# Performance work log

Hardware: AMD Instinct MI355X
Metric: run time of the kernel (lower is better)

## Reference

```python
import jax, jax.numpy as jnp
import numpy as np

N_NODES = 40000
N_EDGES = 640000
D = 128
BN_EPS = 1e-5
GATE_EPS = 1e-6


def _linear_params(key, d_in, d_out):
    kw, kb = jax.random.split(key)
    bound = 1.0 / np.sqrt(d_in)
    W = jax.random.uniform(kw, (d_out, d_in), jnp.float32, -bound, bound)
    b = jax.random.uniform(kb, (d_out,), jnp.float32, -bound, bound)
    return W, b


def setup_inputs() -> dict:
    key = jax.random.key(0)
    ks = jax.random.split(key, 8)
    x = jax.random.normal(ks[0], (N_NODES, D), jnp.float32)
    edge_index = jax.random.randint(ks[1], (2, N_EDGES), 0, N_NODES, jnp.int64)
    edge_attr = jax.random.normal(ks[2], (N_EDGES, D), jnp.float32)
    W_src_gate, b_src_gate = _linear_params(ks[3], D, D)
    W_dst_gate, b_dst_gate = _linear_params(ks[4], D, D)
    W_edge_gate, b_edge_gate = _linear_params(ks[5], D, D)
    W_src_update, b_src_update = _linear_params(ks[6], D, D)
    W_dst_update, b_dst_update = _linear_params(ks[7], D, D)
    return dict(
        x=x, edge_index=edge_index, edge_attr=edge_attr,
        W_src_gate=W_src_gate, b_src_gate=b_src_gate,
        W_dst_gate=W_dst_gate, b_dst_gate=b_dst_gate,
        W_edge_gate=W_edge_gate, b_edge_gate=b_edge_gate,
        W_src_update=W_src_update, b_src_update=b_src_update,
        W_dst_update=W_dst_update, b_dst_update=b_dst_update,
        bn_nodes_gamma=jnp.ones((D,), jnp.float32), bn_nodes_beta=jnp.zeros((D,), jnp.float32),
        bn_edges_gamma=jnp.ones((D,), jnp.float32), bn_edges_beta=jnp.zeros((D,), jnp.float32),
    )


def _batch_norm(z, gamma, beta):
    # training-mode BN: batch mean, biased variance (torch semantics)
    mean = jnp.mean(z, axis=0)
    var = jnp.mean(jnp.square(z - mean), axis=0)
    return gamma * (z - mean) * jax.lax.rsqrt(var + BN_EPS) + beta


def reference(x, edge_index, edge_attr,
              W_src_gate, b_src_gate, W_dst_gate, b_dst_gate,
              W_edge_gate, b_edge_gate, W_src_update, b_src_update,
              W_dst_update, b_dst_update,
              bn_nodes_gamma, bn_nodes_beta, bn_edges_gamma, bn_edges_beta):
    row, col = edge_index[0], edge_index[1]
    num_nodes = x.shape[0]
    x_row = x[row]                      # [E, D] gather
    x_col = x[col]                      # [E, D] gather
    e_src = x_row @ W_src_gate.T + b_src_gate
    e_dst = x_col @ W_dst_gate.T + b_dst_gate
    m = e_src + e_dst + edge_attr @ W_edge_gate.T + b_edge_gate  # [E, D]
    sigma = jax.nn.sigmoid(m)
    h_weighted = (x_col @ W_dst_update.T + b_dst_update) * sigma
    h_sum = jax.ops.segment_sum(h_weighted, col, num_segments=num_nodes)
    sigma_sum = jax.ops.segment_sum(sigma, col, num_segments=num_nodes)
    h_normalized = h_sum / (sigma_sum + GATE_EPS)
    x_new = x @ W_src_update.T + b_src_update + h_normalized
    x_new = jax.nn.softplus(_batch_norm(x_new, bn_nodes_gamma, bn_nodes_beta))
    y_new = jax.nn.softplus(_batch_norm(m, bn_edges_gamma, bn_edges_beta))
    x_new = x + x_new          # residual
    y_new = edge_attr + y_new  # residual
    return (x_new, y_new)
```

## Files before the change

### kernel.cpp

```cpp
#include <hip/hip_runtime.h>

#define NN 40000
#define NE 640000

typedef unsigned short u16;
typedef unsigned int u32;
typedef __attribute__((ext_vector_type(4))) float f32x4;
typedef __attribute__((ext_vector_type(4))) float fv4;
typedef __attribute__((ext_vector_type(4))) u32 uv4;
typedef __attribute__((ext_vector_type(8))) __bf16 bf16x8;

#define LSTR 132
#define TPW 8

__device__ __forceinline__ float bf2f(u16 u) { return __uint_as_float(((u32)u) << 16); }
__device__ __forceinline__ u16 f2bf(float f) {
  u32 u = __float_as_uint(f);
  u32 r = 0x7fffu + ((u >> 16) & 1u);
  return (u16)((u + r) >> 16);
}
__device__ __forceinline__ float splus(float v) {
  return fmaxf(v, 0.0f) + __logf(1.0f + __expf(-fabsf(v)));
}

__global__ void sniff_k(const u32* __restrict__ gamma, const u32* __restrict__ eidx,
                        u32* __restrict__ flags) {
  if (threadIdx.x == 0) {
    flags[0] = (gamma[0] == 0x3F803F80u) ? 1u : 0u;
    u32 odd = eidx[1] | eidx[3] | eidx[5] | eidx[7] |
              eidx[9] | eidx[11] | eidx[13] | eidx[15];
    flags[1] = (odd == 0u) ? 1u : 0u;
  }
}

__device__ __forceinline__ int load_col(const void* eidx, int e, u32 i64) {
  int nc = i64 ? (int)((const u32*)eidx)[2 * ((size_t)NE + e)]
               : ((const int*)eidx)[NE + e];
  return min(max(nc, 0), NN - 1);
}
__device__ __forceinline__ int load_row(const void* eidx, int e, u32 i64) {
  int nr = i64 ? (int)((const u32*)eidx)[2 * (size_t)e]
               : ((const int*)eidx)[e];
  return min(max(nr, 0), NN - 1);
}

__global__ __launch_bounds__(256) void wconv5_k(
    const float* __restrict__ W0, const float* __restrict__ W1,
    const float* __restrict__ W2, const float* __restrict__ W3,
    const float* __restrict__ W4, u16* __restrict__ out) {
  int i = blockIdx.x * 256 + threadIdx.x;
  int mtx = blockIdx.y;
  const float* W = (mtx == 0) ? W0 : (mtx == 1) ? W1 : (mtx == 2) ? W2
                 : (mtx == 3) ? W3 : W4;
  out[mtx * 16384 + i] = f2bf(W[i]);
}

__global__ __launch_bounds__(256) void hist_k(const void* __restrict__ eidx,
                                              u32* __restrict__ cnt,
                                              const u32* __restrict__ flags) {
  int e = blockIdx.x * 256 + threadIdx.x;
  atomicAdd(&cnt[load_col(eidx, e, flags[1])], 1u);
}

__device__ __forceinline__ bf16x8 a_frag(const float* __restrict__ row, int kbase) {
  float4 f0 = *(const float4*)(row + kbase);
  float4 f1 = *(const float4*)(row + kbase + 4);
  bf16x8 a;
  a[0] = (__bf16)f0.x; a[1] = (__bf16)f0.y; a[2] = (__bf16)f0.z; a[3] = (__bf16)f0.w;
  a[4] = (__bf16)f1.x; a[5] = (__bf16)f1.y; a[6] = (__bf16)f1.z; a[7] = (__bf16)f1.w;
  return a;
}

__device__ __forceinline__ bf16x8 cvt8v(fv4 a, fv4 b) {
  bf16x8 r;
  r[0] = (__bf16)a[0]; r[1] = (__bf16)a[1]; r[2] = (__bf16)a[2]; r[3] = (__bf16)a[3];
  r[4] = (__bf16)b[0]; r[5] = (__bf16)b[1]; r[6] = (__bf16)b[2]; r[7] = (__bf16)b[3];
  return r;
}

__device__ __forceinline__ void gemm16(const bf16x8 af[4], const u16* __restrict__ Wb,
                                       const float* __restrict__ bias, int lane,
                                       f32x4 acc[8]) {
  int l15 = lane & 15, lk = lane >> 4;
#pragma unroll
  for (int n = 0; n < 8; ++n) {
    float bv = bias[n * 16 + l15];
    acc[n] = (f32x4){bv, bv, bv, bv};
  }
#pragma unroll
  for (int n = 0; n < 8; ++n) {
    const u16* bp = Wb + (size_t)(n * 16 + l15) * 128 + lk * 8;
#pragma unroll
    for (int k = 0; k < 4; ++k) {
      bf16x8 b = *(const bf16x8*)(bp + 32 * k);
      acc[n] = __builtin_amdgcn_mfma_f32_16x16x32_bf16(af[k], b, acc[n], 0, 0, 0);
    }
  }
}

__device__ __forceinline__ void store_tile(u16* __restrict__ out, int m0, int lane,
                                           const f32x4 acc[8]) {
  int l15 = lane & 15, lk = lane >> 4;
#pragma unroll
  for (int n = 0; n < 8; ++n)
#pragma unroll
    for (int r = 0; r < 4; ++r)
      out[(size_t)(m0 + lk * 4 + r) * 128 + n * 16 + l15] = f2bf(acc[n][r]);
}

__global__ __launch_bounds__(256) void node_gemm_k(
    const float* __restrict__ x, const u16* __restrict__ Wb,
    const float* __restrict__ B0, const float* __restrict__ B1,
    const float* __restrict__ B2, const float* __restrict__ B3,
    const u32* __restrict__ cnt,
    u16* __restrict__ o0, u16* __restrict__ o1,
    u16* __restrict__ o2, u16* __restrict__ o3,
    float* __restrict__ statsg) {
  __shared__ float red[256];
  int tid = threadIdx.x, lane = tid & 63, w = tid >> 6;
  for (int i = tid; i < 256; i += 256) red[i] = 0.f;
  __syncthreads();
  int m0 = blockIdx.x * 64 + w * 16;
  int l15 = lane & 15, lk = lane >> 4;
  const float* arow = x + (size_t)(m0 + l15) * 128;
  bf16x8 af[4];
#pragma unroll
  for (int k = 0; k < 4; ++k) af[k] = a_frag(arow, 32 * k + 8 * lk);
  f32x4 acc[8], accd[8];
  gemm16(af, Wb + 0 * 16384, B0, lane, acc);  store_tile(o0, m0, lane, acc);
  gemm16(af, Wb + 1 * 16384, B1, lane, acc);  store_tile(o1, m0, lane, acc);
  gemm16(af, Wb + 2 * 16384, B2, lane, accd); store_tile(o2, m0, lane, accd);
  gemm16(af, Wb + 3 * 16384, B3, lane, acc);  store_tile(o3, m0, lane, acc);
  float g[4];
#pragma unroll
  for (int r = 0; r < 4; ++r) g[r] = (cnt[m0 + lk * 4 + r] != 0u) ? 1.0f : 0.0f;
#pragma unroll
  for (int n = 0; n < 8; ++n) {
    float a1 = 0.f, a2 = 0.f;
#pragma unroll
    for (int r = 0; r < 4; ++r) {
      float zv = acc[n][r] + g[r] * accd[n][r];
      a1 += zv;
      a2 = fmaf(zv, zv, a2);
    }
    a1 += __shfl_xor(a1, 16); a1 += __shfl_xor(a1, 32);
    a2 += __shfl_xor(a2, 16); a2 += __shfl_xor(a2, 32);
    if (lk == 0) {
      atomicAdd(&red[n * 16 + l15], a1);
      atomicAdd(&red[128 + n * 16 + l15], a2);
    }
  }
  __syncthreads();
  for (int i = tid; i < 256; i += 256) atomicAdd(&statsg[256 + i], red[i]);
}

__global__ __launch_bounds__(256, 2) void edge_gemm_k(
    const float* __restrict__ ea, const u16* __restrict__ Wgb,
    const float* __restrict__ Bg,
    const u16* __restrict__ g_src, const u16* __restrict__ g_dst,
    const void* __restrict__ eidx,
    u16* __restrict__ mge, float* __restrict__ statsg,
    const u32* __restrict__ flags) {
  __shared__ __align__(16) char gbuf[4][16 * LSTR * 4];
  __shared__ __align__(16) u16 Wl[16384];
  int tid = threadIdx.x, lane = tid & 63, w = tid >> 6;
  int l15 = lane & 15, lk = lane >> 4;
  int el = lane >> 2, c4 = lane & 3;
  u32 i64 = flags[1];

  {
    const u32* Wg32 = (const u32*)Wgb;
    u32* Wl32 = (u32*)Wl;
#pragma unroll
    for (int j = 0; j < 32; ++j) {
      int i2 = tid + 256 * j;
      int r = i2 >> 6, c2 = i2 & 63;
      int g = c2 >> 2, win = c2 & 3;
      Wl32[r * 64 + (((g ^ ((r & 7) << 1)) << 2) | win)] = Wg32[i2];
    }
  }
  __syncthreads();

  float* gt = (float*)gbuf[w];
  u16*   mt = (u16*)gbuf[w];
  int sw = (l15 & 7) << 1;

  float bias[8];
#pragma unroll
  for (int n = 0; n < 8; ++n) bias[n] = Bg[n * 16 + l15];

  float e1[8] = {0.f, 0.f, 0.f, 0.f, 0.f, 0.f, 0.f, 0.f};
  float e2[8] = {0.f, 0.f, 0.f, 0.f, 0.f, 0.f, 0.f, 0.f};

  int base = (blockIdx.x * 4 + w) * (TPW * 16);
  const float* aptr = ea + (size_t)(base + l15) * 128 + 8 * lk;

  int rowc = load_row(eidx, base + el, i64);
  int colc = load_col(eidx, base + el, i64);
  fv4 tmp[8];
#pragma unroll
  for (int k = 0; k < 4; ++k) {
    tmp[2 * k]     = *(const fv4*)(aptr + 32 * k);
    tmp[2 * k + 1] = *(const fv4*)(aptr + 32 * k + 4);
  }
  uv4 gsv[2][4], gdv[2][4];
#pragma unroll
  for (int it = 0; it < 4; ++it) {
    gsv[0][it] = *(const uv4*)(g_src + (size_t)rowc * 128 + c4 * 8 + it * 32);
    gdv[0][it] = *(const uv4*)(g_dst + (size_t)colc * 128 + c4 * 8 + it * 32);
  }
  int rown = load_row(eidx, base + 16 + el, i64);
  int coln = load_col(eidx, base + 16 + el, i64);
  bf16x8 af[4];
#pragma unroll
  for (int k = 0; k < 4; ++k) af[k] = cvt8v(tmp[2 * k], tmp[2 * k + 1]);

#pragma unroll
  for (int t = 0; t < TPW; ++t) {
    int cur = t & 1, nxt = cur ^ 1;
    int e0 = base + t * 16;
    if (t + 1 < TPW) {
      const float* anx = aptr + (size_t)(t + 1) * 16 * 128;
#pragma unroll
      for (int k = 0; k < 4; ++k) {
        tmp[2 * k]     = *(const fv4*)(anx + 32 * k);
        tmp[2 * k + 1] = *(const fv4*)(anx + 32 * k + 4);
      }
    }
    if (t + 1 < TPW) {
#pragma unroll
      for (int it = 0; it < 4; ++it) {
        gsv[nxt][it] = *(const uv4*)(g_src + (size_t)rown * 128 + c4 * 8 + it * 32);
        gdv[nxt][it] = *(const uv4*)(g_dst + (size_t)coln * 128 + c4 * 8 + it * 32);
      }
    }
    int rn2 = rown, cn2 = coln;
    if (t + 2 < TPW) {
      rn2 = load_row(eidx, base + (t + 2) * 16 + el, i64);
      cn2 = load_col(eidx, base + (t + 2) * 16 + el, i64);
    }
    f32x4 acc[8];
#pragma unroll
    for (int n = 0; n < 8; ++n)
      acc[n] = (f32x4){bias[n], bias[n], bias[n], bias[n]};
#pragma unroll
    for (int n = 0; n < 8; ++n)
#pragma unroll
      for (int k = 0; k < 4; ++k) {
        bf16x8 b = *(const bf16x8*)(Wl + ((n * 16 + l15) << 7) +
                                    (((lk + 4 * k) ^ sw) << 3));
        acc[n] = __builtin_amdgcn_mfma_f32_16x16x32_bf16(af[k], b, acc[n], 0, 0, 0);
      }
#pragma unroll
    for (int it = 0; it < 4; ++it) {
      const u16* sp = (const u16*)&gsv[cur][it];
      const u16* dp = (const u16*)&gdv[cur][it];
      fv4 lo, hi;
#pragma unroll
      for (int j = 0; j < 4; ++j) lo[j] = bf2f(sp[j]) + bf2f(dp[j]);
#pragma unroll
      for (int j = 0; j < 4; ++j) hi[j] = bf2f(sp[4 + j]) + bf2f(dp[4 + j]);
      int ch = c4 + 4 * it;
      *(fv4*)(gt + el * LSTR + ch * 8)     = lo;
      *(fv4*)(gt + el * LSTR + ch * 8 + 4) = hi;
    }
    float g32[8][4];
#pragma unroll
    for (int n = 0; n < 8; ++n)
#pragma unroll
      for (int r = 0; r < 4; ++r)
        g32[n][r] = gt[(lk * 4 + r) * LSTR + n * 16 + l15];
    __builtin_amdgcn_sched_barrier(0);
#pragma unroll
    for (int n = 0; n < 8; ++n)
#pragma unroll
      for (int r = 0; r < 4; ++r) {
        float mv = acc[n][r] + g32[n][r];
        e1[n] += mv;
        e2[n] = fmaf(mv, mv, e2[n]);
        mt[(lk * 4 + r) * LSTR + n * 16 + l15] = f2bf(mv);
      }
#pragma unroll
    for (int it = 0; it < 4; ++it) {
      int ch = c4 + 4 * it;
      uint4 v = *(const uint4*)(mt + el * LSTR + ch * 8);
      *(uint4*)(mge + (size_t)(e0 + el) * 128 + ch * 8) = v;
    }
    if (t + 1 < TPW) {
#pragma unroll
      for (int k = 0; k < 4; ++k) af[k] = cvt8v(tmp[2 * k], tmp[2 * k + 1]);
    }
    rown = rn2; coln = cn2;
  }
#pragma unroll
  for (int n = 0; n < 8; ++n) {
    float s1 = e1[n], s2 = e2[n];
    s1 += __shfl_xor(s1, 16); s1 += __shfl_xor(s1, 32);
    s2 += __shfl_xor(s2, 16); s2 += __shfl_xor(s2, 32);
    if (lk == 0) {
      atomicAdd(&statsg[n * 16 + l15], s1);
      atomicAdd(&statsg[128 + n * 16 + l15], s2);
    }
  }
}

__global__ void stats_fin_k(const float* __restrict__ es1, const float* __restrict__ es2,
                            const float* __restrict__ ns1, const float* __restrict__ ns2,
                            const float* __restrict__ eg_, const float* __restrict__ eb_,
                            const float* __restrict__ ng_, const float* __restrict__ nb_,
                            float* __restrict__ params) {
  int d = threadIdx.x;
  float em = es1[d] * (1.0f / NE);
  float ev = fmaxf(es2[d] * (1.0f / NE) - em * em, 0.0f);
  float esc = eg_[d] * rsqrtf(ev + 1e-5f);
  params[d] = esc;
  params[128 + d] = eb_[d] - em * esc;
  float nm = ns1[d] * (1.0f / NN);
  float nv = fmaxf(ns2[d] * (1.0f / NN) - nm * nm, 0.0f);
  float nsc = ng_[d] * rsqrtf(nv + 1e-5f);
  params[256 + d] = nsc;
  params[384 + d] = nb_[d] - nm * nsc;
}

__global__ __launch_bounds__(256) void node_fin2_k(
    const float* __restrict__ x, const u16* __restrict__ us,
    const u16* __restrict__ ud, const u32* __restrict__ cnt,
    const float* __restrict__ params, float* __restrict__ out) {
  size_t t = (size_t)blockIdx.x * 256 + threadIdx.x;
  size_t base = t * 8;
  int d0 = (int)(base & 127);
  int n = (int)(t >> 4);
  float g = (cnt[n] != 0u) ? 1.0f : 0.0f;
  float4 xa = *(const float4*)(x + base);
  float4 xb = *(const float4*)(x + base + 4);
  float xv[8] = {xa.x, xa.y, xa.z, xa.w, xb.x, xb.y, xb.z, xb.w};
  uint4 usv = *(const uint4*)(us + base);
  uint4 udv = *(const uint4*)(ud + base);
  const u16* up = (const u16*)&usv;
  const u16* dp = (const u16*)&udv;
  float o[8];
#pragma unroll
  for (int j = 0; j < 8; ++j) {
    float z = bf2f(up[j]) + g * bf2f(dp[j]);
    float bnv = z * params[256 + d0 + j] + params[384 + d0 + j];
    o[j] = xv[j] + splus(bnv);
  }
  *(float4*)(out + base) = make_float4(o[0], o[1], o[2], o[3]);
  *(float4*)(out + base + 4) = make_float4(o[4], o[5], o[6], o[7]);
}

__global__ __launch_bounds__(256) void edge_fin_k(
    const float* __restrict__ edge_attr, const u16* __restrict__ mge,
    const float* __restrict__ params, float* __restrict__ out) {
  size_t t = (size_t)blockIdx.x * 256 + threadIdx.x;
  size_t base = t * 8;
  int d0 = (int)(base & 127);
  float4 ea = *(const float4*)(edge_attr + base);
  float4 eb = *(const float4*)(edge_attr + base + 4);
  float ev[8] = {ea.x, ea.y, ea.z, ea.w, eb.x, eb.y, eb.z, eb.w};
  uint4 mv_ = *(const uint4*)(mge + base);
  const u16* mp = (const u16*)&mv_;
  float o[8];
#pragma unroll
  for (int j = 0; j < 8; ++j) {
    float m = bf2f(mp[j]);
    float bnv = m * params[d0 + j] + params[128 + d0 + j];
    o[j] = ev[j] + splus(bnv);
  }
  *(float4*)(out + base) = make_float4(o[0], o[1], o[2], o[3]);
  *(float4*)(out + base + 4) = make_float4(o[4], o[5], o[6], o[7]);
}

extern "C" void kernel_launch(void* const* d_in, const int* in_sizes, int n_in,
                              void* d_out, int out_size, void* d_ws, size_t ws_size,
                              hipStream_t stream) {
  const float* x        = (const float*)d_in[0];
  const void*  eidx     = d_in[1];
  const float* edge_att = (const float*)d_in[2];
  const float* Wsg = (const float*)d_in[3];  const float* bsg = (const float*)d_in[4];
  const float* Wdg = (const float*)d_in[5];  const float* bdg = (const float*)d_in[6];
  const float* Weg = (const float*)d_in[7];  const float* beg = (const float*)d_in[8];
  const float* Wsu = (const float*)d_in[9];  const float* bsu = (const float*)d_in[10];
  const float* Wdu = (const float*)d_in[11]; const float* bdu = (const float*)d_in[12];
  const float* bng = (const float*)d_in[13]; const float* bnb = (const float*)d_in[14];
  const float* beg_g = (const float*)d_in[15]; const float* beb = (const float*)d_in[16];

  char* ws = (char*)d_ws;
  u16*   g_src  = (u16*)(ws + 0);
  u16*   g_dst  = (u16*)(ws + 10240000);
  u16*   u_dst  = (u16*)(ws + 20480000);
  u16*   u_src  = (u16*)(ws + 30720000);
  float* stats  = (float*)(ws + 40960000);
  u32*   flags  = (u32*)(ws + 40964096);
  u16*   wbuf   = (u16*)(ws + 40968192);
  u32*   cnt    = (u32*)(ws + 41132032);
  u16*   mge    = (u16*)(ws + 41292032);

  hipMemsetAsync(stats, 0, 4096, stream);
  hipMemsetAsync(cnt, 0, 160000, stream);

  sniff_k<<<1, 64, 0, stream>>>((const u32*)bng, (const u32*)eidx, flags);
  wconv5_k<<<dim3(64, 5), 256, 0, stream>>>(Wsg, Wdg, Wdu, Wsu, Weg, wbuf);
  hist_k<<<NE / 256, 256, 0, stream>>>(eidx, cnt, flags);
  node_gemm_k<<<NN / 64, 256, 0, stream>>>(x, wbuf, bsg, bdg, bdu, bsu, cnt,
                                           g_src, g_dst, u_dst, u_src, stats);
  edge_gemm_k<<<NE / (64 * TPW), 256, 0, stream>>>(edge_att, wbuf + 4 * 16384, beg,
                                                   g_src, g_dst, eidx,
                                                   mge, stats, flags);
  stats_fin_k<<<1, 128, 0, stream>>>(stats, stats + 128, stats + 256, stats + 384,
                                     beg_g, beb, bng, bnb, stats + 512);
  node_fin2_k<<<(NN * 128) / 2048, 256, 0, stream>>>(x, u_src, u_dst, cnt,
                                                     stats + 512, (float*)d_out);
  edge_fin_k<<<(NE * 128) / 2048, 256, 0, stream>>>(edge_att, mge, stats + 512,
                                                    (float*)d_out + (size_t)NN * 128);
}
```

Measured before the change: 554.1 us.

## Stage gathered gate sum as bf16 in LDS and raise edge GEMM occupancy

The edge GEMM kernel now adds the src and dst gate rows into a bf16 LDS tile before the MFMAs, then reads, updates and writes that tile in place. This replaces the fp32 staging buffer and the separate bf16 output buffer, which halves per-wave LDS. It also drops the double-buffered gather registers and the full unroll of the tile loop, and raises launch bounds to 3 blocks per CU. The aim is more resident waves to hide gather latency, at the cost of less prefetch distance for the gathers and an extra bf16 rounding of the gate sum before it is added.

```diff
diff --git a/kernel.cpp b/kernel.cpp
--- a/kernel.cpp
+++ b/kernel.cpp
@@ -10,7 +10,7 @@
 typedef __attribute__((ext_vector_type(4))) u32 uv4;
 typedef __attribute__((ext_vector_type(8))) __bf16 bf16x8;
 
-#define LSTR 132
+#define LSTR 136
 #define TPW 8
 
 __device__ __forceinline__ float bf2f(u16 u) { return __uint_as_float(((u32)u) << 16); }
@@ -154,14 +154,14 @@
   for (int i = tid; i < 256; i += 256) atomicAdd(&statsg[256 + i], red[i]);
 }
 
-__global__ __launch_bounds__(256, 2) void edge_gemm_k(
+__global__ __launch_bounds__(256, 3) void edge_gemm_k(
     const float* __restrict__ ea, const u16* __restrict__ Wgb,
     const float* __restrict__ Bg,
     const u16* __restrict__ g_src, const u16* __restrict__ g_dst,
     const void* __restrict__ eidx,
     u16* __restrict__ mge, float* __restrict__ statsg,
     const u32* __restrict__ flags) {
-  __shared__ __align__(16) char gbuf[4][16 * LSTR * 4];
+  __shared__ __align__(16) u16 gbuf[4][16 * LSTR];
   __shared__ __align__(16) u16 Wl[16384];
   int tid = threadIdx.x, lane = tid & 63, w = tid >> 6;
   int l15 = lane & 15, lk = lane >> 4;
@@ -181,8 +181,7 @@
   }
   __syncthreads();
 
-  float* gt = (float*)gbuf[w];
-  u16*   mt = (u16*)gbuf[w];
+  u16* gt = gbuf[w];
   int sw = (l15 & 7) << 1;
 
   float bias[8];
@@ -203,22 +202,34 @@
     tmp[2 * k]     = *(const fv4*)(aptr + 32 * k);
     tmp[2 * k + 1] = *(const fv4*)(aptr + 32 * k + 4);
   }
-  uv4 gsv[2][4], gdv[2][4];
+  uv4 gsv[4], gdv[4];
 #pragma unroll
   for (int it = 0; it < 4; ++it) {
-    gsv[0][it] = *(const uv4*)(g_src + (size_t)rowc * 128 + c4 * 8 + it * 32);
-    gdv[0][it] = *(const uv4*)(g_dst + (size_t)colc * 128 + c4 * 8 + it * 32);
+    gsv[it] = *(const uv4*)(g_src + (size_t)rowc * 128 + c4 * 8 + it * 32);
+    gdv[it] = *(const uv4*)(g_dst + (size_t)colc * 128 + c4 * 8 + it * 32);
   }
   int rown = load_row(eidx, base + 16 + el, i64);
   int coln = load_col(eidx, base + 16 + el, i64);
-  bf16x8 af[4];
-#pragma unroll
-  for (int k = 0; k < 4; ++k) af[k] = cvt8v(tmp[2 * k], tmp[2 * k + 1]);
-
-#pragma unroll
+
   for (int t = 0; t < TPW; ++t) {
-    int cur = t & 1, nxt = cur ^ 1;
     int e0 = base + t * 16;
+#pragma unroll
+    for (int it = 0; it < 4; ++it) {
+      const u16* sp = (const u16*)&gsv[it];
+      const u16* dp = (const u16*)&gdv[it];
+      u32 pk[4];
+#pragma unroll
+      for (int j = 0; j < 4; ++j) {
+        u16 a = f2bf(bf2f(sp[2 * j]) + bf2f(dp[2 * j]));
+        u16 b = f2bf(bf2f(sp[2 * j + 1]) + bf2f(dp[2 * j + 1]));
+        pk[j] = (u32)a | ((u32)b << 16);
+      }
+      int ch = c4 + 4 * it;
+      *(uint4*)(gt + el * LSTR + ch * 8) = make_uint4(pk[0], pk[1], pk[2], pk[3]);
+    }
+    bf16x8 af[4];
+#pragma unroll
+    for (int k = 0; k < 4; ++k) af[k] = cvt8v(tmp[2 * k], tmp[2 * k + 1]);
     if (t + 1 < TPW) {
       const float* anx = aptr + (size_t)(t + 1) * 16 * 128;
 #pragma unroll
@@ -230,8 +241,8 @@
     if (t + 1 < TPW) {
 #pragma unroll
       for (int it = 0; it < 4; ++it) {
-        gsv[nxt][it] = *(const uv4*)(g_src + (size_t)rown * 128 + c4 * 8 + it * 32);
-        gdv[nxt][it] = *(const uv4*)(g_dst + (size_t)coln * 128 + c4 * 8 + it * 32);
+        gsv[it] = *(const uv4*)(g_src + (size_t)rown * 128 + c4 * 8 + it * 32);
+        gdv[it] = *(const uv4*)(g_dst + (size_t)coln * 128 + c4 * 8 + it * 32);
       }
     }
     int rn2 = rown, cn2 = coln;
@@ -252,43 +263,20 @@
         acc[n] = __builtin_amdgcn_mfma_f32_16x16x32_bf16(af[k], b, acc[n], 0, 0, 0);
       }
 #pragma unroll
-    for (int it = 0; it < 4; ++it) {
-      const u16* sp = (const u16*)&gsv[cur][it];
-      const u16* dp = (const u16*)&gdv[cur][it];
-      fv4 lo, hi;
-#pragma unroll
-      for (int j = 0; j < 4; ++j) lo[j] = bf2f(sp[j]) + bf2f(dp[j]);
-#pragma unroll
-      for (int j = 0; j < 4; ++j) hi[j] = bf2f(sp[4 + j]) + bf2f(dp[4 + j]);
-      int ch = c4 + 4 * it;
-      *(fv4*)(gt + el * LSTR + ch * 8)     = lo;
-      *(fv4*)(gt + el * LSTR + ch * 8 + 4) = hi;
-    }
-    float g32[8][4];
-#pragma unroll
     for (int n = 0; n < 8; ++n)
 #pragma unroll
-      for (int r = 0; r < 4; ++r)
-        g32[n][r] = gt[(lk * 4 + r) * LSTR + n * 16 + l15];
-    __builtin_amdgcn_sched_barrier(0);
-#pragma unroll
-    for (int n = 0; n < 8; ++n)
-#pragma unroll
       for (int r = 0; r < 4; ++r) {
-        float mv = acc[n][r] + g32[n][r];
+        int ix = (lk * 4 + r) * LSTR + n * 16 + l15;
+        float mv = acc[n][r] + bf2f(gt[ix]);
         e1[n] += mv;
         e2[n] = fmaf(mv, mv, e2[n]);
-        mt[(lk * 4 + r) * LSTR + n * 16 + l15] = f2bf(mv);
+        gt[ix] = f2bf(mv);
       }
 #pragma unroll
     for (int it = 0; it < 4; ++it) {
       int ch = c4 + 4 * it;
-      uint4 v = *(const uint4*)(mt + el * LSTR + ch * 8);
+      uint4 v = *(const uint4*)(gt + el * LSTR + ch * 8);
       *(uint4*)(mge + (size_t)(e0 + el) * 128 + ch * 8) = v;
-    }
-    if (t + 1 < TPW) {
-#pragma unroll
-      for (int k = 0; k < 4; ++k) af[k] = cvt8v(tmp[2 * k], tmp[2 * k + 1]);
     }
     rown = rn2; coln = cn2;
   }
```

Measured after the change: 681.8 us. +23.1%, slower.
